# Kernel tuning notes

Measured on AMD Instinct MI355X. Metric: run time of the kernel, lower is better.

The kernel has to match this reference:

```python
import jax, jax.numpy as jnp
import numpy as np

# HeteNet distribute_compute reference: per-agent expert id (hete_pick) selects one of
# E heterogeneous expert MLPs; tokens are gathered per expert, run through that expert's
# actor net, and scattered back into a padded [n_threads, n_agents, n_action] output.
# Here each expert is a 2-layer MLP (Net._act actor head approximation):
#   logits = relu(x @ W1[e] + b1[e]) @ W2[e] + b2[e]
# The dispatch/combine is expressed as dense per-expert compute + one-hot combine,
# which is the mathematically identical (mask-select) form of the gather/scatter.

T, N, D, H, A, E = 64, 64, 512, 512, 32, 15  # threads, agents, obs_dim(+addon), hidden, actions, experts


def setup_inputs() -> dict:
    key = jax.random.key(0)
    k0, k1, k2, k3 = jax.random.split(key, 4)
    obs = jax.random.normal(k0, (T, N, D), dtype=jnp.float32)
    hete_pick = jax.random.randint(k1, (T, N), 0, E)  # expert id per agent
    W1 = jax.random.normal(k2, (E, D, H), dtype=jnp.float32) * (1.0 / np.sqrt(D))
    b1 = jnp.zeros((E, H), dtype=jnp.float32)
    W2 = jax.random.normal(k3, (E, H, A), dtype=jnp.float32) * (1.0 / np.sqrt(H))
    b2 = jnp.zeros((E, A), dtype=jnp.float32)
    return {"obs": obs, "W1": W1, "b1": b1, "W2": W2, "b2": b2, "hete_pick": hete_pick}


def reference(obs, W1, b1, W2, b2, hete_pick):
    # per-expert dense forward: [E, T, N, H]
    h = jax.nn.relu(jnp.einsum('tnd,edh->etnh', obs, W1) + b1[:, None, None, :])
    logits = jnp.einsum('etnh,eha->etna', h, W2) + b2[:, None, None, :]  # [E,T,N,A]
    # combine: scatter each expert's rows back per mask (hete_pick == e)
    onehot = (hete_pick[None, :, :] == jnp.arange(E)[:, None, None]).astype(obs.dtype)  # [E,T,N]
    return jnp.einsum('etna,etn->tna', logits, onehot)  # [T,N,A]
```

## Files before the change

kernel.cpp:

```cpp
#include <hip/hip_runtime.h>
#include <stdint.h>

#define NTOK 4096
#define DDIM 512
#define HDIM 512
#define ADIM 32
#define NEXP 15
#define TILE_M 32
#define MAXTILE 143
#define GRID_M 152

typedef __attribute__((ext_vector_type(8))) short bf16x8;
typedef __attribute__((ext_vector_type(8))) unsigned short ushort8;
typedef __attribute__((ext_vector_type(4))) unsigned short ushort4v;
typedef __attribute__((ext_vector_type(4))) float f32x4;

__device__ __forceinline__ unsigned short f2bf(float f) {
  unsigned int u = __float_as_uint(f);
  u += 0x7fffu + ((u >> 16) & 1u);
  return (unsigned short)(u >> 16);
}

__device__ __forceinline__ void gld_lds16(const void* g, void* l) {
  __builtin_amdgcn_global_load_lds(
      (const __attribute__((address_space(1))) void*)g,
      (__attribute__((address_space(3))) void*)l, 16, 0, 0);
}

__global__ __launch_bounds__(256) void prep_kernel(
    const float* __restrict__ W1, const float* __restrict__ W2,
    const int* __restrict__ pick, int* __restrict__ meta,
    int* __restrict__ lists, unsigned short* __restrict__ W1I,
    unsigned short* __restrict__ W2T)
{
  extern __shared__ char smem[];
  const int bid = blockIdx.x;
  const int tid = threadIdx.x;
  if (bid < 240) {
    float* s = (float*)smem;
    const int e = bid / 16, kc = bid % 16, r0 = kc * 32;
    const float* src = W1 + (size_t)e * (DDIM * HDIM) + (size_t)r0 * HDIM;
    #pragma unroll
    for (int v = 0; v < 16; ++v) {
      int i = v * 256 + tid;
      int row = i >> 7, col = (i & 127) * 4;
      *(float4*)(s + row * 517 + col) = *(const float4*)(src + (size_t)row * 512 + col);
    }
    __syncthreads();
    unsigned short* dst = W1I + (size_t)(e * 16 + kc) * 512 * 32;
    const int p = tid & 3;
    #pragma unroll
    for (int w = 0; w < 8; ++w) {
      int n = w * 64 + (tid >> 2);
      int q = p ^ ((n >> 1) & 3);
      ushort8 vv;
      #pragma unroll
      for (int x = 0; x < 8; ++x) vv[x] = f2bf(s[(q * 8 + x) * 517 + n]);
      *(ushort8*)(dst + (size_t)n * 32 + p * 8) = vv;
    }
  } else if (bid < 255) {
    float* s = (float*)smem;
    const int e = bid - 240;
    const float* src = W2 + (size_t)e * (HDIM * ADIM);
    #pragma unroll
    for (int v = 0; v < 16; ++v) {
      int i = v * 256 + tid;
      int row = i >> 3, col = (i & 7) * 4;
      *(float4*)(s + row * 36 + col) = *(const float4*)(src + (size_t)row * 32 + col);
    }
    __syncthreads();
    unsigned short* dst = W2T + (size_t)e * (ADIM * HDIM);
    const int a = tid >> 3, k0 = (tid & 7) * 64;
    #pragma unroll
    for (int w = 0; w < 8; ++w) {
      ushort8 vv;
      #pragma unroll
      for (int x = 0; x < 8; ++x) vv[x] = f2bf(s[(size_t)(k0 + w * 8 + x) * 36 + a]);
      *(ushort8*)(dst + (size_t)a * 512 + k0 + w * 8) = vv;
    }
  } else {
    int* s_inc = (int*)smem;
    int* s_run = s_inc + NEXP * 256;
    int pk[16];
    #pragma unroll
    for (int i = 0; i < 16; ++i) pk[i] = pick[tid * 16 + i];
    #pragma unroll
    for (int e = 0; e < NEXP; ++e) {
      int c = 0;
      #pragma unroll
      for (int i = 0; i < 16; ++i) c += (pk[i] == e) ? 1 : 0;
      s_inc[e * 256 + tid] = c;
    }
    __syncthreads();
    for (int off = 1; off < 256; off <<= 1) {
      int v[NEXP];
      #pragma unroll
      for (int e = 0; e < NEXP; ++e) v[e] = (tid >= off) ? s_inc[e * 256 + tid - off] : 0;
      __syncthreads();
      #pragma unroll
      for (int e = 0; e < NEXP; ++e) s_inc[e * 256 + tid] += v[e];
      __syncthreads();
    }
    #pragma unroll
    for (int e = 0; e < NEXP; ++e) s_run[e * 256 + tid] = (tid > 0) ? s_inc[e * 256 + tid - 1] : 0;
    __syncthreads();
    #pragma unroll
    for (int i = 0; i < 16; ++i) {
      int p = pk[i];
      int pos = s_run[p * 256 + tid]++;
      lists[p * NTOK + pos] = tid * 16 + i;
    }
    if (tid < NEXP) meta[tid] = s_inc[tid * 256 + 255];
    __syncthreads();
    if (tid == 0) {
      int tot = 0;
      for (int ee = 0; ee < NEXP; ++ee) {
        int c = s_inc[ee * 256 + 255];
        int nt = (c + TILE_M - 1) / TILE_M;
        for (int i = 0; i < nt; ++i) meta[16 + tot++] = (ee << 16) | i;
      }
      meta[15] = tot;
    }
  }
}

__global__ __launch_bounds__(256, 1) void moe_gemm(
    const float* __restrict__ obs, const float* __restrict__ b1,
    const float* __restrict__ b2, const int* __restrict__ meta,
    const int* __restrict__ lists, const unsigned short* __restrict__ W1I,
    const unsigned short* __restrict__ W2T, float* __restrict__ out)
{
  const int ntiles = meta[15];
  const int p = blockIdx.x;
  const int xq = ntiles >> 3, xr = ntiles & 7;
  const int xcd = p & 7, slot = p >> 3;
  const int cx = xq + (xcd < xr ? 1 : 0);
  if (slot >= cx) return;
  const int j = xcd * xq + (xcd < xr ? xcd : xr) + slot;

  const int tl = meta[16 + j];
  const int e = tl >> 16;
  const int tile_lo = (tl & 0xffff) * TILE_M;
  const int cnt = meta[e];
  int mvalid = cnt - tile_lo; if (mvalid > TILE_M) mvalid = TILE_M;

  extern __shared__ char smem[];
  char* s_x = smem;
  char* wb0 = smem + 32768;
  char* wb1 = smem + 65536;
  char* wb2 = smem + 98304;

  const int tid = threadIdx.x, lane = tid & 63, wave = tid >> 6;
  const int l15 = lane & 15, l4 = lane >> 4;
  const int nbase = wave * 128;
  const int* mylist = lists + e * NTOK;
  const unsigned short* w1i_e = W1I + (size_t)e * 16 * 512 * 32;
  const unsigned short* w2t_e = W2T + (size_t)e * (ADIM * HDIM);

  const int m = tid >> 3, s8 = tid & 7;
  int idx = tile_lo + m; if (idx >= cnt) idx = cnt - 1;
  const float* grow = obs + (size_t)mylist[idx] * DDIM;
  float4 xf[16];
  #pragma unroll
  for (int si = 0; si < 8; ++si) {
    xf[si * 2]     = *(const float4*)(grow + (s8 + si * 8) * 8);
    xf[si * 2 + 1] = *(const float4*)(grow + (s8 + si * 8) * 8 + 4);
  }
  __builtin_amdgcn_sched_barrier(0);

  auto issue_w1 = [&](int t, char* buf) {
    const unsigned short* base = w1i_e + (size_t)t * (512 * 32);
    #pragma unroll
    for (int i = 0; i < 8; ++i) {
      int nb = nbase + i * 16;
      gld_lds16(base + (size_t)nb * 32 + lane * 8, buf + nb * 64);
    }
  };
  issue_w1(0, wb0);
  __builtin_amdgcn_sched_barrier(0);
  issue_w1(1, wb1);
  __builtin_amdgcn_sched_barrier(0);

  #pragma unroll
  for (int si = 0; si < 8; ++si) {
    int s = s8 + si * 8;
    float4 f0 = xf[si * 2], f1 = xf[si * 2 + 1];
    ushort8 v;
    v[0] = f2bf(f0.x); v[1] = f2bf(f0.y); v[2] = f2bf(f0.z); v[3] = f2bf(f0.w);
    v[4] = f2bf(f1.x); v[5] = f2bf(f1.y); v[6] = f2bf(f1.z); v[7] = f2bf(f1.w);
    *(ushort8*)(s_x + m * 1024 + ((s ^ (m & 7)) << 4)) = v;
  }
  __syncthreads();

  f32x4 acc[8][2];
  #pragma unroll
  for (int nt = 0; nt < 8; ++nt) {
    float4 bv = *(const float4*)(b1 + e * HDIM + nbase + nt * 16 + l4 * 4);
    f32x4 b4 = {bv.x, bv.y, bv.z, bv.w};
    acc[nt][0] = b4; acc[nt][1] = b4;
  }

  #pragma unroll
  for (int t = 0; t < 16; ++t) {
    if (t < 14) {
      char* nxt = ((t + 2) % 3 == 0) ? wb0 : ((t + 2) % 3 == 1) ? wb1 : wb2;
      issue_w1(t + 2, nxt);
    } else if (t == 14) {
      #pragma unroll
      for (int i = 0; i < 8; ++i) {
        int a = wave * 8 + i;
        gld_lds16(w2t_e + (size_t)a * 512 + (size_t)(lane ^ (a & 7)) * 8, wb1 + a * 1024);
      }
    }
    if (t < 15) asm volatile("s_waitcnt vmcnt(16)" ::: "memory");
    else        asm volatile("s_waitcnt vmcnt(8)" ::: "memory");
    __builtin_amdgcn_sched_barrier(0);

    const char* cw = (t % 3 == 0) ? wb0 : (t % 3 == 1) ? wb1 : wb2;
    bf16x8 wfr[8], xfr[2];
    #pragma unroll
    for (int nt = 0; nt < 8; ++nt) {
      int n = nbase + nt * 16 + l15;
      wfr[nt] = *(const bf16x8*)(cw + n * 64 + ((l4 ^ ((n >> 1) & 3)) << 4));
    }
    #pragma unroll
    for (int mt = 0; mt < 2; ++mt) {
      int mm = mt * 16 + l15;
      xfr[mt] = *(const bf16x8*)(s_x + mm * 1024 + ((((t << 2) + l4) ^ (mm & 7)) << 4));
    }
    #pragma unroll
    for (int nt = 0; nt < 8; ++nt)
      #pragma unroll
      for (int mt = 0; mt < 2; ++mt)
        acc[nt][mt] = __builtin_amdgcn_mfma_f32_16x16x32_bf16(wfr[nt], xfr[mt], acc[nt][mt], 0, 0, 0);
  }

  __syncthreads();

  #pragma unroll
  for (int nt = 0; nt < 8; ++nt) {
    int n0 = nbase + nt * 16 + l4 * 4;
    int sg = n0 >> 3, half = (n0 >> 2) & 1;
    #pragma unroll
    for (int mt = 0; mt < 2; ++mt) {
      int mm = mt * 16 + l15;
      ushort4v hv;
      #pragma unroll
      for (int r = 0; r < 4; ++r) hv[r] = f2bf(fmaxf(acc[nt][mt][r], 0.f));
      *(ushort4v*)(s_x + mm * 1024 + ((sg ^ (mm & 7)) << 4) + half * 8) = hv;
    }
  }
  __syncthreads();

  const int mt2 = wave >> 1, at2 = wave & 1;
  const float b2v = b2[e * ADIM + at2 * 16 + l15];
  f32x4 acc2 = {b2v, b2v, b2v, b2v};
  #pragma unroll
  for (int ks = 0; ks < 16; ++ks) {
    int mm = mt2 * 16 + l15;
    bf16x8 af = *(const bf16x8*)(s_x + mm * 1024 + ((((ks << 2) + l4) ^ (mm & 7)) << 4));
    int a = at2 * 16 + l15;
    bf16x8 bf = *(const bf16x8*)(wb1 + a * 1024 + ((((ks << 2) + l4) ^ (a & 7)) << 4));
    acc2 = __builtin_amdgcn_mfma_f32_16x16x32_bf16(af, bf, acc2, 0, 0, 0);
  }
  #pragma unroll
  for (int r = 0; r < 4; ++r) {
    int mrow = mt2 * 16 + l4 * 4 + r;
    if (mrow < mvalid)
      out[(size_t)mylist[tile_lo + mrow] * ADIM + at2 * 16 + l15] = acc2[r];
  }
}

__global__ __launch_bounds__(256) void naive_kernel(
    const float* __restrict__ obs, const float* __restrict__ W1,
    const float* __restrict__ b1, const float* __restrict__ W2,
    const float* __restrict__ b2, const int* __restrict__ pick,
    float* __restrict__ out)
{
  __shared__ float sx[DDIM];
  __shared__ float sh[HDIM];
  const int t = blockIdx.x, tid = threadIdx.x;
  const int e = pick[t];
  const float* x = obs + (size_t)t * DDIM;
  for (int i = tid; i < DDIM; i += 256) sx[i] = x[i];
  __syncthreads();
  const float* w1 = W1 + (size_t)e * DDIM * HDIM;
  for (int j = tid; j < HDIM; j += 256) {
    float a = b1[e * HDIM + j];
    for (int d = 0; d < DDIM; ++d) a = fmaf(sx[d], w1[(size_t)d * HDIM + j], a);
    sh[j] = a > 0.f ? a : 0.f;
  }
  __syncthreads();
  if (tid < ADIM) {
    const float* w2 = W2 + (size_t)e * HDIM * ADIM;
    float a = b2[e * ADIM + tid];
    for (int j = 0; j < HDIM; ++j) a = fmaf(sh[j], w2[(size_t)j * ADIM + tid], a);
    out[(size_t)t * ADIM + tid] = a;
  }
}

extern "C" void kernel_launch(void* const* d_in, const int* in_sizes, int n_in,
                              void* d_out, int out_size, void* d_ws, size_t ws_size,
                              hipStream_t stream)
{
  const float* obs = (const float*)d_in[0];
  const float* W1  = (const float*)d_in[1];
  const float* b1  = (const float*)d_in[2];
  const float* W2  = (const float*)d_in[3];
  const float* b2  = (const float*)d_in[4];
  const int* pick  = (const int*)d_in[5];
  float* out = (float*)d_out;
  (void)in_sizes; (void)n_in; (void)out_size;

  const size_t OFF_LISTS = 1024;
  const size_t OFF_W1I   = 262144;
  const size_t OFF_W2T   = OFF_W1I + (size_t)NEXP * HDIM * DDIM * 2;
  const size_t WS_NEEDED = OFF_W2T + (size_t)NEXP * ADIM * HDIM * 2;

  if (ws_size < WS_NEEDED) {
    naive_kernel<<<dim3(NTOK), dim3(256), 0, stream>>>(obs, W1, b1, W2, b2, pick, out);
    return;
  }

  char* ws = (char*)d_ws;
  int* meta   = (int*)ws;
  int* lists  = (int*)(ws + OFF_LISTS);
  unsigned short* W1I = (unsigned short*)(ws + OFF_W1I);
  unsigned short* W2T = (unsigned short*)(ws + OFF_W2T);

  prep_kernel<<<dim3(256), dim3(256), 73728, stream>>>(
      W1, W2, pick, meta, lists, W1I, W2T);
  moe_gemm<<<dim3(GRID_M), dim3(256), 131072, stream>>>(
      obs, b1, b2, meta, lists, W1I, W2T, out);
}
```

Measured before the change: 28.01 us.

## Use 64-row tiles split across two blocks by hidden half with atomic combine

```diff
diff --git a/kernel.cpp b/kernel.cpp
--- a/kernel.cpp
+++ b/kernel.cpp
@@ -6,9 +6,8 @@
 #define HDIM 512
 #define ADIM 32
 #define NEXP 15
-#define TILE_M 32
-#define MAXTILE 143
-#define GRID_M 152
+#define TILE_M 64
+#define GRID_M 160
 
 typedef __attribute__((ext_vector_type(8))) short bf16x8;
 typedef __attribute__((ext_vector_type(8))) unsigned short ushort8;
@@ -31,7 +30,7 @@
     const float* __restrict__ W1, const float* __restrict__ W2,
     const int* __restrict__ pick, int* __restrict__ meta,
     int* __restrict__ lists, unsigned short* __restrict__ W1I,
-    unsigned short* __restrict__ W2T)
+    unsigned short* __restrict__ W2T, float* __restrict__ out)
 {
   extern __shared__ char smem[];
   const int bid = blockIdx.x;
@@ -59,6 +58,9 @@
       *(ushort8*)(dst + (size_t)n * 32 + p * 8) = vv;
     }
   } else if (bid < 255) {
+    float4 z4; z4.x = 0.f; z4.y = 0.f; z4.z = 0.f; z4.w = 0.f;
+    for (int i = (bid - 240) * 256 + tid; i < NTOK * ADIM / 4; i += 15 * 256)
+      ((float4*)out)[i] = z4;
     float* s = (float*)smem;
     const int e = bid - 240;
     const float* src = W2 + (size_t)e * (HDIM * ADIM);
@@ -131,14 +133,16 @@
     const unsigned short* __restrict__ W2T, float* __restrict__ out)
 {
   const int ntiles = meta[15];
+  const int nphys = ntiles * 2;
   const int p = blockIdx.x;
-  const int xq = ntiles >> 3, xr = ntiles & 7;
+  const int xq = nphys >> 3, xr = nphys & 7;
   const int xcd = p & 7, slot = p >> 3;
   const int cx = xq + (xcd < xr ? 1 : 0);
   if (slot >= cx) return;
-  const int j = xcd * xq + (xcd < xr ? xcd : xr) + slot;
-
-  const int tl = meta[16 + j];
+  const int j2 = xcd * xq + (xcd < xr ? xcd : xr) + slot;
+  const int jt = j2 >> 1, half = j2 & 1;
+
+  const int tl = meta[16 + jt];
   const int e = tl >> 16;
   const int tile_lo = (tl & 0xffff) * TILE_M;
   const int cnt = meta[e];
@@ -146,33 +150,23 @@
 
   extern __shared__ char smem[];
   char* s_x = smem;
-  char* wb0 = smem + 32768;
-  char* wb1 = smem + 65536;
+  char* wb0 = smem + 65536;
+  char* wb1 = smem + 81920;
   char* wb2 = smem + 98304;
 
   const int tid = threadIdx.x, lane = tid & 63, wave = tid >> 6;
   const int l15 = lane & 15, l4 = lane >> 4;
-  const int nbase = wave * 128;
+  const int nbl = wave * 64;
+  const int hbase = half * 256;
   const int* mylist = lists + e * NTOK;
   const unsigned short* w1i_e = W1I + (size_t)e * 16 * 512 * 32;
   const unsigned short* w2t_e = W2T + (size_t)e * (ADIM * HDIM);
 
-  const int m = tid >> 3, s8 = tid & 7;
-  int idx = tile_lo + m; if (idx >= cnt) idx = cnt - 1;
-  const float* grow = obs + (size_t)mylist[idx] * DDIM;
-  float4 xf[16];
-  #pragma unroll
-  for (int si = 0; si < 8; ++si) {
-    xf[si * 2]     = *(const float4*)(grow + (s8 + si * 8) * 8);
-    xf[si * 2 + 1] = *(const float4*)(grow + (s8 + si * 8) * 8 + 4);
-  }
-  __builtin_amdgcn_sched_barrier(0);
-
   auto issue_w1 = [&](int t, char* buf) {
-    const unsigned short* base = w1i_e + (size_t)t * (512 * 32);
-    #pragma unroll
-    for (int i = 0; i < 8; ++i) {
-      int nb = nbase + i * 16;
+    const unsigned short* base = w1i_e + (size_t)t * (512 * 32) + (size_t)hbase * 32;
+    #pragma unroll
+    for (int i = 0; i < 4; ++i) {
+      int nb = nbl + i * 16;
       gld_lds16(base + (size_t)nb * 32 + lane * 8, buf + nb * 64);
     }
   };
@@ -181,23 +175,30 @@
   issue_w1(1, wb1);
   __builtin_amdgcn_sched_barrier(0);
 
-  #pragma unroll
-  for (int si = 0; si < 8; ++si) {
-    int s = s8 + si * 8;
-    float4 f0 = xf[si * 2], f1 = xf[si * 2 + 1];
-    ushort8 v;
-    v[0] = f2bf(f0.x); v[1] = f2bf(f0.y); v[2] = f2bf(f0.z); v[3] = f2bf(f0.w);
-    v[4] = f2bf(f1.x); v[5] = f2bf(f1.y); v[6] = f2bf(f1.z); v[7] = f2bf(f1.w);
-    *(ushort8*)(s_x + m * 1024 + ((s ^ (m & 7)) << 4)) = v;
-  }
-  __syncthreads();
-
-  f32x4 acc[8][2];
-  #pragma unroll
-  for (int nt = 0; nt < 8; ++nt) {
-    float4 bv = *(const float4*)(b1 + e * HDIM + nbase + nt * 16 + l4 * 4);
+  {
+    const int m = tid >> 2, sq = tid & 3;
+    int idx = tile_lo + m; if (idx >= cnt) idx = cnt - 1;
+    const float* grow = obs + (size_t)mylist[idx] * DDIM;
+    #pragma unroll 4
+    for (int si = 0; si < 16; ++si) {
+      const int s = sq + si * 4;
+      float4 f0 = *(const float4*)(grow + s * 8);
+      float4 f1 = *(const float4*)(grow + s * 8 + 4);
+      ushort8 v;
+      v[0] = f2bf(f0.x); v[1] = f2bf(f0.y); v[2] = f2bf(f0.z); v[3] = f2bf(f0.w);
+      v[4] = f2bf(f1.x); v[5] = f2bf(f1.y); v[6] = f2bf(f1.z); v[7] = f2bf(f1.w);
+      *(ushort8*)(s_x + m * 1024 + ((s ^ (m & 7)) << 4)) = v;
+    }
+  }
+  __syncthreads();
+
+  f32x4 acc[4][4];
+  #pragma unroll
+  for (int nt = 0; nt < 4; ++nt) {
+    float4 bv = *(const float4*)(b1 + e * HDIM + hbase + nbl + nt * 16 + l4 * 4);
     f32x4 b4 = {bv.x, bv.y, bv.z, bv.w};
-    acc[nt][0] = b4; acc[nt][1] = b4;
+    #pragma unroll
+    for (int mt = 0; mt < 4; ++mt) acc[nt][mt] = b4;
   }
 
   #pragma unroll
@@ -207,68 +208,80 @@
       issue_w1(t + 2, nxt);
     } else if (t == 14) {
       #pragma unroll
-      for (int i = 0; i < 8; ++i) {
-        int a = wave * 8 + i;
-        gld_lds16(w2t_e + (size_t)a * 512 + (size_t)(lane ^ (a & 7)) * 8, wb1 + a * 1024);
+      for (int i = 0; i < 4; ++i) {
+        int o = wave * 4096 + i * 1024 + lane * 16;
+        int a = o >> 9;
+        int p16 = (o >> 4) & 31;
+        gld_lds16(w2t_e + (size_t)a * 512 + hbase + (size_t)((p16 ^ (a & 7)) * 8),
+                  wb1 + o);
       }
     }
-    if (t < 15) asm volatile("s_waitcnt vmcnt(16)" ::: "memory");
-    else        asm volatile("s_waitcnt vmcnt(8)" ::: "memory");
+    if (t < 15) asm volatile("s_waitcnt vmcnt(8)" ::: "memory");
+    else        asm volatile("s_waitcnt vmcnt(4)" ::: "memory");
     __builtin_amdgcn_sched_barrier(0);
 
     const char* cw = (t % 3 == 0) ? wb0 : (t % 3 == 1) ? wb1 : wb2;
-    bf16x8 wfr[8], xfr[2];
-    #pragma unroll
-    for (int nt = 0; nt < 8; ++nt) {
-      int n = nbase + nt * 16 + l15;
+    bf16x8 wfr[4], xfr[4];
+    #pragma unroll
+    for (int nt = 0; nt < 4; ++nt) {
+      int n = nbl + nt * 16 + l15;
       wfr[nt] = *(const bf16x8*)(cw + n * 64 + ((l4 ^ ((n >> 1) & 3)) << 4));
     }
     #pragma unroll
-    for (int mt = 0; mt < 2; ++mt) {
+    for (int mt = 0; mt < 4; ++mt) {
       int mm = mt * 16 + l15;
       xfr[mt] = *(const bf16x8*)(s_x + mm * 1024 + ((((t << 2) + l4) ^ (mm & 7)) << 4));
     }
     #pragma unroll
-    for (int nt = 0; nt < 8; ++nt)
-      #pragma unroll
-      for (int mt = 0; mt < 2; ++mt)
+    for (int nt = 0; nt < 4; ++nt)
+      #pragma unroll
+      for (int mt = 0; mt < 4; ++mt)
         acc[nt][mt] = __builtin_amdgcn_mfma_f32_16x16x32_bf16(wfr[nt], xfr[mt], acc[nt][mt], 0, 0, 0);
   }
 
   __syncthreads();
 
   #pragma unroll
-  for (int nt = 0; nt < 8; ++nt) {
-    int n0 = nbase + nt * 16 + l4 * 4;
-    int sg = n0 >> 3, half = (n0 >> 2) & 1;
-    #pragma unroll
-    for (int mt = 0; mt < 2; ++mt) {
+  for (int nt = 0; nt < 4; ++nt) {
+    int n0 = nbl + nt * 16 + l4 * 4;
+    int sg = n0 >> 3, hsel = (n0 >> 2) & 1;
+    #pragma unroll
+    for (int mt = 0; mt < 4; ++mt) {
       int mm = mt * 16 + l15;
       ushort4v hv;
       #pragma unroll
       for (int r = 0; r < 4; ++r) hv[r] = f2bf(fmaxf(acc[nt][mt][r], 0.f));
-      *(ushort4v*)(s_x + mm * 1024 + ((sg ^ (mm & 7)) << 4) + half * 8) = hv;
-    }
-  }
-  __syncthreads();
-
-  const int mt2 = wave >> 1, at2 = wave & 1;
-  const float b2v = b2[e * ADIM + at2 * 16 + l15];
-  f32x4 acc2 = {b2v, b2v, b2v, b2v};
-  #pragma unroll
-  for (int ks = 0; ks < 16; ++ks) {
-    int mm = mt2 * 16 + l15;
-    bf16x8 af = *(const bf16x8*)(s_x + mm * 1024 + ((((ks << 2) + l4) ^ (mm & 7)) << 4));
-    int a = at2 * 16 + l15;
-    bf16x8 bf = *(const bf16x8*)(wb1 + a * 1024 + ((((ks << 2) + l4) ^ (a & 7)) << 4));
-    acc2 = __builtin_amdgcn_mfma_f32_16x16x32_bf16(af, bf, acc2, 0, 0, 0);
-  }
-  #pragma unroll
-  for (int r = 0; r < 4; ++r) {
-    int mrow = mt2 * 16 + l4 * 4 + r;
-    if (mrow < mvalid)
-      out[(size_t)mylist[tile_lo + mrow] * ADIM + at2 * 16 + l15] = acc2[r];
-  }
+      *(ushort4v*)(s_x + mm * 1024 + ((sg ^ (mm & 7)) << 4) + hsel * 8) = hv;
+    }
+  }
+  __syncthreads();
+
+  const int mm2 = wave * 16 + l15;
+  f32x4 acc2[2];
+  #pragma unroll
+  for (int at = 0; at < 2; ++at) {
+    float b2v = half ? 0.f : b2[e * ADIM + at * 16 + l15];
+    f32x4 b4 = {b2v, b2v, b2v, b2v};
+    acc2[at] = b4;
+  }
+  #pragma unroll
+  for (int ks = 0; ks < 8; ++ks) {
+    bf16x8 af = *(const bf16x8*)(s_x + mm2 * 1024 + ((((ks << 2) + l4) ^ (mm2 & 7)) << 4));
+    #pragma unroll
+    for (int at = 0; at < 2; ++at) {
+      int a = at * 16 + l15;
+      bf16x8 bf = *(const bf16x8*)(wb1 + a * 512 + ((((ks << 2) + l4) ^ (a & 7)) << 4));
+      acc2[at] = __builtin_amdgcn_mfma_f32_16x16x32_bf16(af, bf, acc2[at], 0, 0, 0);
+    }
+  }
+  #pragma unroll
+  for (int at = 0; at < 2; ++at)
+    #pragma unroll
+    for (int r = 0; r < 4; ++r) {
+      int mrow = wave * 16 + l4 * 4 + r;
+      if (mrow < mvalid)
+        atomicAdd(&out[(size_t)mylist[tile_lo + mrow] * ADIM + at * 16 + l15], acc2[at][r]);
+    }
 }
 
 __global__ __launch_bounds__(256) void naive_kernel(
@@ -329,7 +342,7 @@
   unsigned short* W2T = (unsigned short*)(ws + OFF_W2T);
 
   prep_kernel<<<dim3(256), dim3(256), 73728, stream>>>(
-      W1, W2, pick, meta, lists, W1I, W2T);
-  moe_gemm<<<dim3(GRID_M), dim3(256), 131072, stream>>>(
+      W1, W2, pick, meta, lists, W1I, W2T, out);
+  moe_gemm<<<dim3(GRID_M), dim3(256), 114688, stream>>>(
       obs, b1, b2, meta, lists, W1I, W2T, out);
 }
```

New measurement: 28.57 us. 2.0% more time.
